# Optimization experiments

Hardware: AMD Instinct MI355X
Metric: run time of the kernel (lower is better)

## Reference

```python
import jax, jax.numpy as jnp
import numpy as np

NT = 3            # node types
NET = 9           # edge types = all ordered pairs
PAIR_A = np.repeat(np.arange(NT), NT)   # et[0].value per edge type
PAIR_B = np.tile(np.arange(NT), NT)     # et[1].value per edge type


def setup_inputs() -> dict:
    key = jax.random.key(0)
    ks = jax.random.split(key, 20)
    bs, Na, Nc, CS, D, H, Z = 8, 128, 256, 3, 64, 64, 8
    s = 0.05
    inp = {
        'node_types': jax.random.randint(ks[0], (bs, Na), 0, NT),
        'node_enc': jax.random.normal(ks[1], (bs, Na, D), dtype=jnp.float32),
        'edge_enc': jax.random.normal(ks[2], (bs, Na, Na, 1, D), dtype=jnp.float32),
        'clique_index': jax.random.randint(ks[3], (bs, Nc), 0, Na),
        'clique_node_index': jax.random.randint(ks[4], (bs, Nc, CS), 0, Na),
        'clique_order_index': jax.random.randint(ks[5], (bs, Nc, CS), 0, CS),
        # per-node-type MLP params (stacked over type axis)
        'nW0': jax.random.normal(ks[6], (NT, D, H)) * s, 'nb0': jnp.zeros((NT, H)),
        'nW1': jax.random.normal(ks[7], (NT, H, H)) * s, 'nb1': jnp.zeros((NT, H)),
        'nW2': jax.random.normal(ks[8], (NT, H, Z)) * s, 'nb2': jnp.zeros((NT, Z)),
        # per-edge-type MLP params
        'eW0': jax.random.normal(ks[9], (NET, D, H)) * s, 'eb0': jnp.zeros((NET, H)),
        'eW1': jax.random.normal(ks[10], (NET, H, H)) * s, 'eb1': jnp.zeros((NET, H)),
        'eW2': jax.random.normal(ks[11], (NET, H, Z * Z)) * s, 'eb2': jnp.zeros((NET, Z * Z)),
    }
    return inp


def reference(node_types, node_enc, edge_enc, clique_index, clique_node_index,
              clique_order_index, nW0, nb0, nW1, nb1, nW2, nb2,
              eW0, eb0, eW1, eb1, eW2, eb2):
    bs, Na = node_types.shape
    Nc, cs = clique_node_index.shape[1:]
    Z = nb2.shape[-1]

    # ---- node factors: dense per-type MLP then type-mask accumulate ----
    h = jax.nn.relu(jnp.einsum('bnd,tdh->tbnh', node_enc, nW0) + nb0[:, None, None, :])
    h = jax.nn.relu(jnp.einsum('tbnh,thk->tbnk', h, nW1) + nb1[:, None, None, :])
    nf_all = jnp.einsum('tbnk,tkz->tbnz', h, nW2) + nb2[:, None, None, :]  # [T,bs,Na,Z]
    nmask = (node_types[None] == jnp.arange(NT)[:, None, None]).astype(nf_all.dtype)
    node_factor = jnp.einsum('tbnz,tbn->bnz', nf_all, nmask)  # [bs,Na,Z]

    # ---- edge factors: last timestep of edge_enc, per-pair-type MLP + mask ----
    e = edge_enc[..., -1, :]  # [bs,Na,Na,D]
    h = jax.nn.relu(jnp.einsum('bijd,tdh->tbijh', e, eW0) + eb0[:, None, None, None, :])
    h = jax.nn.relu(jnp.einsum('tbijh,thk->tbijk', h, eW1) + eb1[:, None, None, None, :])
    ef_all = jnp.einsum('tbijk,tkz->tbijz', h, eW2) + eb2[:, None, None, None, :]  # [9,bs,Na,Na,Z*Z]
    pa = jnp.asarray(PAIR_A)
    pb = jnp.asarray(PAIR_B)
    # et_flag[b,i,j] = (types[b,j]==et0) & (types[b,i]==et1)  (matches torch unsqueeze(1)/(2))
    emask = ((node_types[None, :, None, :] == pa[:, None, None, None]) &
             (node_types[None, :, :, None] == pb[:, None, None, None])).astype(ef_all.dtype)
    edge_factor = jnp.einsum('tbijz,tbij->bijz', ef_all, emask).reshape(bs, Na, Na, Z, Z)

    # ---- pad with zero row/col for index -1 sentinel ----
    nfe = jnp.pad(node_factor, ((0, 0), (0, 1), (0, 0)))                     # [bs,Na+1,Z]
    efe = jnp.pad(edge_factor, ((0, 0), (0, 1), (0, 1), (0, 0), (0, 0)))
    efe_flat = efe.reshape(bs, (Na + 1) * (Na + 1), Z, Z)

    idx = jnp.where(clique_node_index < 0, Na, clique_node_index)  # [bs,Nc,cs]
    b_ix = jnp.arange(bs)[:, None, None]
    nfc = nfe[b_ix, idx]  # [bs,Nc,cs,Z]

    logpi = jnp.zeros((bs, Nc) + (Z,) * cs, node_factor.dtype)
    for i in range(cs):
        shape = (bs, Nc) + (1,) * i + (Z,) + (1,) * (cs - 1 - i)
        logpi = logpi + nfc[:, :, i, :].reshape(shape)
    b2 = jnp.arange(bs)[:, None]
    for i in range(cs - 1):
        for j in range(i + 1, cs):
            fl = idx[:, :, i] * (Na + 1) + idx[:, :, j]          # [bs,Nc]
            ef_ij = efe_flat[b2, fl]                              # [bs,Nc,Z,Z]
            shape = (bs, Nc) + (1,) * i + (Z,) + (1,) * (j - i - 1) + (Z,) + (1,) * (cs - 1 - j)
            logpi = logpi + ef_ij.reshape(shape)

    z = jnp.stack(jnp.meshgrid(*([jnp.arange(Z)] * cs), indexing='ij'), -1)
    return logpi, z
```

## Files before the change

kernel.cpp:

```cpp
#include <hip/hip_runtime.h>
#include <hip/hip_bf16.h>


#define BS   8
#define NA   128
#define NC   256
#define DIM  64
#define ZZ   8

#define WS_EF_OFF (BS * NA * ZZ)

__global__ __launch_bounds__(256) void node_mlp_kernel(
    const int* __restrict__ nt, const float* __restrict__ enc,
    const float* __restrict__ W0, const float* __restrict__ b0,
    const float* __restrict__ W1, const float* __restrict__ b1,
    const float* __restrict__ W2, const float* __restrict__ b2,
    float* __restrict__ nf) {
  const int blk = blockIdx.x;
  const int tid = threadIdx.x;
  const int j = tid & 63, s = tid >> 6;
  const int t = nt[blk];

  __shared__ float e[DIM];
  __shared__ float h[DIM];
  __shared__ float red[4][DIM];
  __shared__ float red2[8][ZZ];

  if (tid < DIM) e[tid] = enc[blk * DIM + tid];
  __syncthreads();

  {
    float a = 0.f;
    const float* w = W0 + t * DIM * DIM + s * 16 * DIM + j;
#pragma unroll
    for (int k = 0; k < 16; ++k) a = fmaf(e[s * 16 + k], w[k * DIM], a);
    red[s][j] = a;
  }
  __syncthreads();
  if (s == 0) {
    float v = red[0][j] + red[1][j] + red[2][j] + red[3][j] + b0[t * DIM + j];
    h[j] = fmaxf(v, 0.f);
  }
  __syncthreads();

  {
    float a = 0.f;
    const float* w = W1 + t * DIM * DIM + s * 16 * DIM + j;
#pragma unroll
    for (int k = 0; k < 16; ++k) a = fmaf(h[s * 16 + k], w[k * DIM], a);
    red[s][j] = a;
  }
  __syncthreads();
  if (s == 0) {
    float v = red[0][j] + red[1][j] + red[2][j] + red[3][j] + b1[t * DIM + j];
    e[j] = fmaxf(v, 0.f);
  }
  __syncthreads();

  if (tid < DIM) {
    const int j2 = tid & 7, s2 = tid >> 3;
    float a = 0.f;
    const float* w = W2 + t * DIM * ZZ + s2 * 8 * ZZ + j2;
#pragma unroll
    for (int k = 0; k < 8; ++k) a = fmaf(e[s2 * 8 + k], w[k * ZZ], a);
    red2[s2][j2] = a;
  }
  __syncthreads();
  if (tid < ZZ) {
    float v = b2[t * ZZ + tid];
#pragma unroll
    for (int s2 = 0; s2 < 8; ++s2) v += red2[s2][tid];
    nf[blk * ZZ + tid] = v;
  }
}

__global__ __launch_bounds__(256) void edge_mlp_kernel(
    const int* __restrict__ nt, const int* __restrict__ cni,
    const float* __restrict__ edge_enc,
    const float* __restrict__ eW0, const float* __restrict__ eb0,
    const float* __restrict__ eW1, const float* __restrict__ eb1,
    const float* __restrict__ eW2, const float* __restrict__ eb2,
    float* __restrict__ ef_out) {
  const int blk = blockIdx.x;
  const int tid = threadIdx.x;
  const int j = tid & 63, s = tid >> 6;
  const int clique = blk / 3, pair = blk - clique * 3;
  const int b = clique >> 8;

  const int pi = (pair == 2) ? 1 : 0;
  const int pj = (pair == 0) ? 1 : 2;

  __shared__ int idxs[2];
  __shared__ float e[DIM];
  __shared__ float h[DIM];
  __shared__ float red[4][DIM];

  if (tid == 0) {
    int va = cni[clique * 3 + pi];
    int vb = cni[clique * 3 + pj];
    idxs[0] = (va < 0 || va >= NA) ? NA : va;
    idxs[1] = (vb < 0 || vb >= NA) ? NA : vb;
  }
  __syncthreads();
  const int ia = idxs[0], jb = idxs[1];

  if (ia >= NA || jb >= NA) {
    if (tid < DIM) ef_out[blk * DIM + tid] = 0.f;
    return;
  }
  const int t = nt[b * NA + jb] * 3 + nt[b * NA + ia];

  if (tid < DIM) e[tid] = edge_enc[((b * NA + ia) * NA + jb) * DIM + tid];
  __syncthreads();

  {
    float a = 0.f;
    const float* w = eW0 + t * DIM * DIM + s * 16 * DIM + j;
#pragma unroll
    for (int k = 0; k < 16; ++k) a = fmaf(e[s * 16 + k], w[k * DIM], a);
    red[s][j] = a;
  }
  __syncthreads();
  if (s == 0) {
    float v = red[0][j] + red[1][j] + red[2][j] + red[3][j] + eb0[t * DIM + j];
    h[j] = fmaxf(v, 0.f);
  }
  __syncthreads();

  {
    float a = 0.f;
    const float* w = eW1 + t * DIM * DIM + s * 16 * DIM + j;
#pragma unroll
    for (int k = 0; k < 16; ++k) a = fmaf(h[s * 16 + k], w[k * DIM], a);
    red[s][j] = a;
  }
  __syncthreads();
  if (s == 0) {
    float v = red[0][j] + red[1][j] + red[2][j] + red[3][j] + eb1[t * DIM + j];
    e[j] = fmaxf(v, 0.f);
  }
  __syncthreads();

  {
    float a = 0.f;
    const float* w = eW2 + t * DIM * DIM + s * 16 * DIM + j;
#pragma unroll
    for (int k = 0; k < 16; ++k) a = fmaf(e[s * 16 + k], w[k * DIM], a);
    red[s][j] = a;
  }
  __syncthreads();
  if (s == 0) {
    ef_out[blk * DIM + j] =
        red[0][j] + red[1][j] + red[2][j] + red[3][j] + eb2[t * DIM + j];
  }
}

__global__ __launch_bounds__(64) void assemble_kernel(
    const int* __restrict__ cni, const float* __restrict__ nf,
    const float* __restrict__ ef_in, float* __restrict__ out) {
  const int blk = blockIdx.x;
  const int lane = threadIdx.x;
  const int b = blk >> 8;

  __shared__ int idxs[3];
  __shared__ float nfs[3][ZZ];
  __shared__ float ef[3][DIM];

  if (lane < 3) {
    int v = cni[blk * 3 + lane];
    idxs[lane] = (v < 0 || v >= NA) ? NA : v;
  }
  __syncthreads();
  if (lane < 3 * ZZ) {
    const int i = lane >> 3, z = lane & 7;
    const int v = idxs[i];
    nfs[i][z] = (v < NA) ? nf[(b * NA + v) * ZZ + z] : 0.f;
  }
#pragma unroll
  for (int p = 0; p < 3; ++p) ef[p][lane] = ef_in[(blk * 3 + p) * DIM + lane];
  __syncthreads();

  const int z1 = lane >> 3, z2 = lane & 7;
  const float base = nfs[1][z1] + nfs[2][z2] + ef[2][z1 * ZZ + z2];
  float* o = out + blk * (ZZ * ZZ * ZZ);
#pragma unroll
  for (int z0 = 0; z0 < ZZ; ++z0) {
    o[z0 * 64 + lane] = base + nfs[0][z0] + ef[0][z0 * ZZ + z1] + ef[1][z0 * ZZ + z2];
  }

  if (blk < 24) {
    const int i = blk * 64 + lane;
    const int k = i % 3;
    const int r = i / 3;
    const int zz2 = r & 7, zz1 = (r >> 3) & 7, zz0 = r >> 6;
    const int v = (k == 0) ? zz0 : ((k == 1) ? zz1 : zz2);
    out[BS * NC * ZZ * ZZ * ZZ + i] = (float)v;
  }
}

extern "C" void kernel_launch(void* const* d_in, const int* in_sizes, int n_in,
                              void* d_out, int out_size, void* d_ws, size_t ws_size,
                              hipStream_t stream) {
  const int*   node_types = (const int*)  d_in[0];
  const float* node_enc   = (const float*)d_in[1];
  const float* edge_enc   = (const float*)d_in[2];
  const int*   cni        = (const int*)  d_in[4];
  const float* nW0 = (const float*)d_in[6];
  const float* nb0 = (const float*)d_in[7];
  const float* nW1 = (const float*)d_in[8];
  const float* nb1 = (const float*)d_in[9];
  const float* nW2 = (const float*)d_in[10];
  const float* nb2 = (const float*)d_in[11];
  const float* eW0 = (const float*)d_in[12];
  const float* eb0 = (const float*)d_in[13];
  const float* eW1 = (const float*)d_in[14];
  const float* eb1 = (const float*)d_in[15];
  const float* eW2 = (const float*)d_in[16];
  const float* eb2 = (const float*)d_in[17];

  float* out = (float*)d_out;
  float* node_factor = (float*)d_ws;
  float* ef_buf = (float*)d_ws + WS_EF_OFF;

  node_mlp_kernel<<<BS * NA, 256, 0, stream>>>(
      node_types, node_enc, nW0, nb0, nW1, nb1, nW2, nb2, node_factor);

  edge_mlp_kernel<<<BS * NC * 3, 256, 0, stream>>>(
      node_types, cni, edge_enc, eW0, eb0, eW1, eb1, eW2, eb2, ef_buf);

  assemble_kernel<<<BS * NC, 64, 0, stream>>>(cni, node_factor, ef_buf, out);
}
```

Baseline: 127.1 us.

## Fuse edge MLP with clique assembly using wave-level shuffle matvecs

Merges the edge MLP and assemble kernels into one kernel with one block per clique. Each of three wavefronts runs the MLP for one node pair, and the fourth loads node factors. The matvec now uses register shuffles and float4 weight loads instead of shared-memory reductions and block barriers, and the edge-factor round trip through global workspace and one launch are removed. In exchange, each block does three serial MLPs inside single waves, so there are fewer, longer blocks.

```diff
diff --git a/kernel.cpp b/kernel.cpp
--- a/kernel.cpp
+++ b/kernel.cpp
@@ -1,5 +1,4 @@
 #include <hip/hip_runtime.h>
-#include <hip/hip_bf16.h>
 
 
 #define BS   8
@@ -8,7 +7,6 @@
 #define DIM  64
 #define ZZ   8
 
-#define WS_EF_OFF (BS * NA * ZZ)
 
 __global__ __launch_bounds__(256) void node_mlp_kernel(
     const int* __restrict__ nt, const float* __restrict__ enc,
@@ -74,127 +72,100 @@
   }
 }
 
-__global__ __launch_bounds__(256) void edge_mlp_kernel(
+__device__ __forceinline__ float mv64(float v, const float* __restrict__ W,
+                                      const float* __restrict__ B, int lane,
+                                      bool relu) {
+  const int j4 = (lane & 15) * 4;
+  const int ks = lane >> 4;
+  float ax = 0.f, ay = 0.f, az = 0.f, aw = 0.f;
+#pragma unroll 8
+  for (int i = 0; i < 16; ++i) {
+    const int k = ks * 16 + i;
+    const float vk = __shfl(v, k);
+    const float4 w4 = *reinterpret_cast<const float4*>(W + k * DIM + j4);
+    ax = fmaf(vk, w4.x, ax);
+    ay = fmaf(vk, w4.y, ay);
+    az = fmaf(vk, w4.z, az);
+    aw = fmaf(vk, w4.w, aw);
+  }
+  ax += __shfl_xor(ax, 16); ay += __shfl_xor(ay, 16);
+  az += __shfl_xor(az, 16); aw += __shfl_xor(aw, 16);
+  ax += __shfl_xor(ax, 32); ay += __shfl_xor(ay, 32);
+  az += __shfl_xor(az, 32); aw += __shfl_xor(aw, 32);
+  const int src = lane >> 2;
+  const float s0 = __shfl(ax, src);
+  const float s1 = __shfl(ay, src);
+  const float s2 = __shfl(az, src);
+  const float s3 = __shfl(aw, src);
+  const int c = lane & 3;
+  float r = (c == 0) ? s0 : (c == 1) ? s1 : (c == 2) ? s2 : s3;
+  r += B[lane];
+  return relu ? fmaxf(r, 0.f) : r;
+}
+
+__global__ __launch_bounds__(256) void edge_assemble_kernel(
     const int* __restrict__ nt, const int* __restrict__ cni,
     const float* __restrict__ edge_enc,
     const float* __restrict__ eW0, const float* __restrict__ eb0,
     const float* __restrict__ eW1, const float* __restrict__ eb1,
     const float* __restrict__ eW2, const float* __restrict__ eb2,
-    float* __restrict__ ef_out) {
+    const float* __restrict__ nf, float* __restrict__ out) {
   const int blk = blockIdx.x;
   const int tid = threadIdx.x;
-  const int j = tid & 63, s = tid >> 6;
-  const int clique = blk / 3, pair = blk - clique * 3;
-  const int b = clique >> 8;
-
-  const int pi = (pair == 2) ? 1 : 0;
-  const int pj = (pair == 0) ? 1 : 2;
-
-  __shared__ int idxs[2];
-  __shared__ float e[DIM];
-  __shared__ float h[DIM];
-  __shared__ float red[4][DIM];
-
-  if (tid == 0) {
-    int va = cni[clique * 3 + pi];
-    int vb = cni[clique * 3 + pj];
-    idxs[0] = (va < 0 || va >= NA) ? NA : va;
-    idxs[1] = (vb < 0 || vb >= NA) ? NA : vb;
-  }
-  __syncthreads();
-  const int ia = idxs[0], jb = idxs[1];
-
-  if (ia >= NA || jb >= NA) {
-    if (tid < DIM) ef_out[blk * DIM + tid] = 0.f;
-    return;
-  }
-  const int t = nt[b * NA + jb] * 3 + nt[b * NA + ia];
-
-  if (tid < DIM) e[tid] = edge_enc[((b * NA + ia) * NA + jb) * DIM + tid];
-  __syncthreads();
-
-  {
-    float a = 0.f;
-    const float* w = eW0 + t * DIM * DIM + s * 16 * DIM + j;
-#pragma unroll
-    for (int k = 0; k < 16; ++k) a = fmaf(e[s * 16 + k], w[k * DIM], a);
-    red[s][j] = a;
-  }
-  __syncthreads();
-  if (s == 0) {
-    float v = red[0][j] + red[1][j] + red[2][j] + red[3][j] + eb0[t * DIM + j];
-    h[j] = fmaxf(v, 0.f);
-  }
-  __syncthreads();
-
-  {
-    float a = 0.f;
-    const float* w = eW1 + t * DIM * DIM + s * 16 * DIM + j;
-#pragma unroll
-    for (int k = 0; k < 16; ++k) a = fmaf(h[s * 16 + k], w[k * DIM], a);
-    red[s][j] = a;
-  }
-  __syncthreads();
-  if (s == 0) {
-    float v = red[0][j] + red[1][j] + red[2][j] + red[3][j] + eb1[t * DIM + j];
-    e[j] = fmaxf(v, 0.f);
-  }
-  __syncthreads();
-
-  {
-    float a = 0.f;
-    const float* w = eW2 + t * DIM * DIM + s * 16 * DIM + j;
-#pragma unroll
-    for (int k = 0; k < 16; ++k) a = fmaf(e[s * 16 + k], w[k * DIM], a);
-    red[s][j] = a;
-  }
-  __syncthreads();
-  if (s == 0) {
-    ef_out[blk * DIM + j] =
-        red[0][j] + red[1][j] + red[2][j] + red[3][j] + eb2[t * DIM + j];
-  }
-}
-
-__global__ __launch_bounds__(64) void assemble_kernel(
-    const int* __restrict__ cni, const float* __restrict__ nf,
-    const float* __restrict__ ef_in, float* __restrict__ out) {
-  const int blk = blockIdx.x;
-  const int lane = threadIdx.x;
+  const int lane = tid & 63, wid = tid >> 6;
   const int b = blk >> 8;
 
-  __shared__ int idxs[3];
+  __shared__ float ef_s[3][DIM];
   __shared__ float nfs[3][ZZ];
-  __shared__ float ef[3][DIM];
-
-  if (lane < 3) {
-    int v = cni[blk * 3 + lane];
-    idxs[lane] = (v < 0 || v >= NA) ? NA : v;
-  }
-  __syncthreads();
-  if (lane < 3 * ZZ) {
-    const int i = lane >> 3, z = lane & 7;
-    const int v = idxs[i];
-    nfs[i][z] = (v < NA) ? nf[(b * NA + v) * ZZ + z] : 0.f;
-  }
-#pragma unroll
-  for (int p = 0; p < 3; ++p) ef[p][lane] = ef_in[(blk * 3 + p) * DIM + lane];
-  __syncthreads();
-
-  const int z1 = lane >> 3, z2 = lane & 7;
-  const float base = nfs[1][z1] + nfs[2][z2] + ef[2][z1 * ZZ + z2];
-  float* o = out + blk * (ZZ * ZZ * ZZ);
-#pragma unroll
-  for (int z0 = 0; z0 < ZZ; ++z0) {
-    o[z0 * 64 + lane] = base + nfs[0][z0] + ef[0][z0 * ZZ + z1] + ef[1][z0 * ZZ + z2];
-  }
-
-  if (blk < 24) {
-    const int i = blk * 64 + lane;
-    const int k = i % 3;
-    const int r = i / 3;
-    const int zz2 = r & 7, zz1 = (r >> 3) & 7, zz0 = r >> 6;
-    const int v = (k == 0) ? zz0 : ((k == 1) ? zz1 : zz2);
-    out[BS * NC * ZZ * ZZ * ZZ + i] = (float)v;
+
+  int rawv = (lane < 3) ? cni[blk * 3 + lane] : -1;
+  int ivc = (rawv < 0 || rawv >= NA) ? NA : rawv;
+  int tt = (ivc < NA) ? nt[b * NA + ivc] : 0;
+  const int id0 = __shfl(ivc, 0), id1 = __shfl(ivc, 1), id2 = __shfl(ivc, 2);
+  const int tp0 = __shfl(tt, 0), tp1 = __shfl(tt, 1), tp2 = __shfl(tt, 2);
+
+  if (wid < 3) {
+    const int pi = (wid == 2) ? 1 : 0;
+    const int pj = (wid == 0) ? 1 : 2;
+    const int ia = (pi == 0) ? id0 : id1;
+    const int jb = (pj == 1) ? id1 : id2;
+    float res = 0.f;
+    if (ia < NA && jb < NA) {
+      const int ta = (pi == 0) ? tp0 : tp1;
+      const int tb = (pj == 1) ? tp1 : tp2;
+      const int t = tb * 3 + ta;
+      float v = edge_enc[((size_t)(b * NA + ia) * NA + jb) * DIM + lane];
+      v = mv64(v, eW0 + t * DIM * DIM, eb0 + t * DIM, lane, true);
+      v = mv64(v, eW1 + t * DIM * DIM, eb1 + t * DIM, lane, true);
+      res = mv64(v, eW2 + t * DIM * DIM, eb2 + t * DIM, lane, false);
+    }
+    ef_s[wid][lane] = res;
+  } else if (lane < 3 * ZZ) {
+    const int slot = lane >> 3, z = lane & 7;
+    const int ix = (slot == 0) ? id0 : (slot == 1) ? id1 : id2;
+    nfs[slot][z] = (ix < NA) ? nf[(b * NA + ix) * ZZ + z] : 0.f;
+  }
+  __syncthreads();
+
+  float* o = out + (size_t)blk * (ZZ * ZZ * ZZ);
+#pragma unroll
+  for (int r = 0; r < 2; ++r) {
+    const int i = r * 256 + tid;
+    const int z0 = i >> 6, z1 = (i >> 3) & 7, z2 = i & 7;
+    o[i] = nfs[0][z0] + nfs[1][z1] + nfs[2][z2]
+         + ef_s[0][z0 * ZZ + z1] + ef_s[1][z0 * ZZ + z2] + ef_s[2][z1 * ZZ + z2];
+  }
+
+  if (blk < 3) {
+#pragma unroll
+    for (int r = 0; r < 2; ++r) {
+      const int i = blk * 512 + r * 256 + tid;
+      const int k = i % 3;
+      const int rr = i / 3;
+      const int zz2 = rr & 7, zz1 = (rr >> 3) & 7, zz0 = rr >> 6;
+      out[BS * NC * ZZ * ZZ * ZZ + i] =
+          (float)((k == 0) ? zz0 : (k == 1) ? zz1 : zz2);
+    }
   }
 }
 
@@ -220,13 +191,11 @@
 
   float* out = (float*)d_out;
   float* node_factor = (float*)d_ws;
-  float* ef_buf = (float*)d_ws + WS_EF_OFF;
 
   node_mlp_kernel<<<BS * NA, 256, 0, stream>>>(
       node_types, node_enc, nW0, nb0, nW1, nb1, nW2, nb2, node_factor);
 
-  edge_mlp_kernel<<<BS * NC * 3, 256, 0, stream>>>(
-      node_types, cni, edge_enc, eW0, eb0, eW1, eb1, eW2, eb2, ef_buf);
-
-  assemble_kernel<<<BS * NC, 64, 0, stream>>>(cni, node_factor, ef_buf, out);
-}
+  edge_assemble_kernel<<<BS * NC, 256, 0, stream>>>(
+      node_types, cni, edge_enc, eW0, eb0, eW1, eb1, eW2, eb2,
+      node_factor, out);
+}
```

After: 124.9 us. About the same (-1.8%).
